# Optimization experiments

Measured on AMD Instinct MI355X. Metric: run time of the kernel, lower is better.

The kernel has to match this reference:

```python
import jax, jax.numpy as jnp
import numpy as np

B, N, M, K = 8, 24000, 6000, 32
C_IN, C_MID, C_OUT = 64, 128, 256  # channels=[64,128,256]; conv input is C_IN+3 (dp_fj)


def setup_inputs() -> dict:
    key = jax.random.key(0)
    ks = jax.random.split(key, 8)
    return {
        "query_xyz": jax.random.normal(ks[0], (B, M, 3), jnp.float32),
        "support_xyz": jax.random.normal(ks[1], (B, N, 3), jnp.float32),
        "features": jax.random.normal(ks[2], (B, C_IN, N), jnp.float32),
        "neighbor_idx": jax.random.randint(ks[3], (B, M, K), 0, N, dtype=jnp.int32),
        "W1": jax.random.normal(ks[4], (C_MID, C_IN + 3), jnp.float32) * 0.05,
        "b1": jnp.zeros((C_MID,), jnp.float32),
        "W2": jax.random.normal(ks[5], (C_OUT, C_MID), jnp.float32) * 0.05,
        "b2": jnp.zeros((C_OUT,), jnp.float32),
    }


def _conv1d_relu(x, W, b):
    # pointwise conv1d (kernel size 1) + bias + ReLU; x: [B, Cin, N]
    return jax.nn.relu(jnp.einsum('oc,bcn->bon', W, x) + b[None, :, None])


def reference(query_xyz, support_xyz, features, neighbor_idx, W1, b1, W2, b2):
    # Delayed aggregation: transform features FIRST (convs on support points),
    # then gather neighbors per query and max-reduce.
    x = jnp.concatenate([features, support_xyz.transpose(0, 2, 1)], axis=1)  # [B, C_IN+3, N]
    x = _conv1d_relu(x, W1, b1)   # [B, C_MID, N]
    x = _conv1d_relu(x, W2, b2)   # [B, C_OUT, N]
    # grouper: gather neighbor features fj = x[b, :, neighbor_idx[b, m, k]] -> [B, C_OUT, M, K]
    idx = jnp.broadcast_to(neighbor_idx.reshape(B, 1, M * K), (B, C_OUT, M * K))
    fj = jnp.take_along_axis(x, idx, axis=2).reshape(B, C_OUT, M, K)
    # reduction_layer: max over neighbor dim
    return jnp.max(fj, axis=-1)  # [B, C_OUT, M]
```

## Files before the change

kernel.cpp:

```cpp
#include <hip/hip_runtime.h>
#include <hip/hip_bf16.h>

typedef unsigned short u16;
typedef short s16x8 __attribute__((ext_vector_type(8)));
typedef float f32x4 __attribute__((ext_vector_type(4)));
typedef unsigned short u16x8 __attribute__((ext_vector_type(8)));

#define B_   8
#define N_   24000
#define M_   6000
#define K_   32
#define CIN  64
#define CMID 128
#define COUT 256
#define KP1  96
#define QB_  188

__device__ __align__(16) u16 g_W1f[CMID * KP1];
__device__ __align__(16) u16 g_W2f[COUT * CMID];
__device__ __align__(16) u16 g_Yf[(size_t)B_ * N_ * COUT];

__device__ __forceinline__ float bf2f(u16 u) {
    return __uint_as_float(((unsigned)u) << 16);
}
__device__ __forceinline__ u16 f2bf(float f) {
    unsigned u = __float_as_uint(f);
    u += 0x7FFFu + ((u >> 16) & 1u);
    return (u16)(u >> 16);
}
__device__ __forceinline__ unsigned f2bf2(float lo, float hi) {
    __hip_bfloat162 h = __float22bfloat162_rn(make_float2(lo, hi));
    unsigned r;
    __builtin_memcpy(&r, &h, 4);
    return r;
}

__global__ void prep_weights(const float* __restrict__ W1,
                             const float* __restrict__ W2) {
    int t = blockIdx.x * 256 + threadIdx.x;
    if (t < CMID * KP1) {
        int blk = t >> 9, off = t & 511;
        int L = off >> 3, j = off & 7;
        int ln = L & 15, quad = L >> 4;
        int w = blk / 6, r = blk % 6;
        int k0i = r >> 1, mt = r & 1;
        int row = w * 32 + mt * 16 + ln;
        int col = k0i * 32 + quad * 8 + j;
        g_W1f[t] = (col < 67) ? f2bf(W1[row * 67 + col]) : (u16)0;
    } else {
        int i = t - CMID * KP1;
        int blk = i >> 9, off = i & 511;
        int L = off >> 3, j = off & 7;
        int ln = L & 15, quad = L >> 4;
        int w = blk >> 4, r = blk & 15;
        int k0i = r >> 2, mt = r & 3;
        int row = w * 64 + mt * 16 + ln;
        int col = k0i * 32 + quad * 8 + j;
        g_W2f[i] = f2bf(W2[row * 128 + col]);
    }
}

__global__ __launch_bounds__(256) void conv_fused(
        const float* __restrict__ feat, const float* __restrict__ xyz,
        const float* __restrict__ b1,  const float* __restrict__ b2) {
    __shared__ __align__(16) u16 sm[16896];
    u16* Xs = sm;
    u16* Hs = sm + 6656;
    u16* Ys = sm;

    const int tid  = threadIdx.x;
    const int b    = blockIdx.y;
    const int n0   = blockIdx.x * 64;
    const int w    = tid >> 6;
    const int L    = tid & 63;
    const int ln   = L & 15;
    const int quad = L >> 4;

    if (tid < 64) {
        uint4 z; z.x = z.y = z.z = z.w = 0u;
        u16* xr = Xs + tid * 104;
        *(uint4*)(xr + 64) = z; *(uint4*)(xr + 72) = z;
        *(uint4*)(xr + 80) = z; *(uint4*)(xr + 88) = z;
        const float* s = xyz + (size_t)(b * N_ + n0 + tid) * 3;
        xr[64] = f2bf(s[0]); xr[65] = f2bf(s[1]); xr[66] = f2bf(s[2]);
    }
#pragma unroll
    for (int it = 0; it < 4; ++it) {
        int idx = it * 256 + tid;
        int c   = idx >> 4;
        int p0  = (idx & 15) << 2;
        float4 v = *(const float4*)(feat + (size_t)(b * CIN + c) * N_ + n0 + p0);
        u16* dst = Xs + p0 * 104 + c;
        unsigned pxy = f2bf2(v.x, v.y);
        unsigned pzw = f2bf2(v.z, v.w);
        dst[0]   = (u16)pxy;
        dst[104] = (u16)(pxy >> 16);
        dst[208] = (u16)pzw;
        dst[312] = (u16)(pzw >> 16);
    }
    __syncthreads();

    f32x4 acc1[2][4];
#pragma unroll
    for (int mt = 0; mt < 2; ++mt)
#pragma unroll
        for (int nt = 0; nt < 4; ++nt) {
            f32x4 zz = {0.f, 0.f, 0.f, 0.f};
            acc1[mt][nt] = zz;
        }
#pragma unroll
    for (int k0i = 0; k0i < 3; ++k0i) {
        s16x8 af[2], xf[4];
#pragma unroll
        for (int mt = 0; mt < 2; ++mt)
            af[mt] = *(const s16x8*)(g_W1f + (((w * 3 + k0i) * 2 + mt) << 9) + L * 8);
#pragma unroll
        for (int nt = 0; nt < 4; ++nt)
            xf[nt] = *(const s16x8*)(Xs + (nt * 16 + ln) * 104 + k0i * 32 + quad * 8);
#pragma unroll
        for (int mt = 0; mt < 2; ++mt)
#pragma unroll
            for (int nt = 0; nt < 4; ++nt)
                acc1[mt][nt] = __builtin_amdgcn_mfma_f32_16x16x32_bf16(
                    af[mt], xf[nt], acc1[mt][nt], 0, 0, 0);
    }
#pragma unroll
    for (int mt = 0; mt < 2; ++mt) {
        int m0 = w * 32 + mt * 16 + quad * 4;
        float4 bv = *(const float4*)(b1 + m0);
#pragma unroll
        for (int nt = 0; nt < 4; ++nt) {
            int p = nt * 16 + ln;
            uint2 hv;
            hv.x = f2bf2(fmaxf(acc1[mt][nt][0] + bv.x, 0.f),
                         fmaxf(acc1[mt][nt][1] + bv.y, 0.f));
            hv.y = f2bf2(fmaxf(acc1[mt][nt][2] + bv.z, 0.f),
                         fmaxf(acc1[mt][nt][3] + bv.w, 0.f));
            *(uint2*)(Hs + p * 136 + m0) = hv;
        }
    }
    __syncthreads();

    f32x4 acc2[4][4];
#pragma unroll
    for (int mt = 0; mt < 4; ++mt)
#pragma unroll
        for (int nt = 0; nt < 4; ++nt) {
            f32x4 zz = {0.f, 0.f, 0.f, 0.f};
            acc2[mt][nt] = zz;
        }
#pragma unroll
    for (int k0i = 0; k0i < 4; ++k0i) {
        s16x8 af[4], hf[4];
#pragma unroll
        for (int mt = 0; mt < 4; ++mt)
            af[mt] = *(const s16x8*)(g_W2f + (((w * 4 + k0i) * 4 + mt) << 9) + L * 8);
#pragma unroll
        for (int nt = 0; nt < 4; ++nt)
            hf[nt] = *(const s16x8*)(Hs + (nt * 16 + ln) * 136 + k0i * 32 + quad * 8);
#pragma unroll
        for (int mt = 0; mt < 4; ++mt)
#pragma unroll
            for (int nt = 0; nt < 4; ++nt)
                acc2[mt][nt] = __builtin_amdgcn_mfma_f32_16x16x32_bf16(
                    af[mt], hf[nt], acc2[mt][nt], 0, 0, 0);
    }
    __syncthreads();

#pragma unroll
    for (int mt = 0; mt < 4; ++mt) {
        int c0 = w * 64 + mt * 16 + quad * 4;
        float4 bv = *(const float4*)(b2 + c0);
#pragma unroll
        for (int nt = 0; nt < 4; ++nt) {
            int p = nt * 16 + ln;
            uint2 yv;
            yv.x = f2bf2(fmaxf(acc2[mt][nt][0] + bv.x, 0.f),
                         fmaxf(acc2[mt][nt][1] + bv.y, 0.f));
            yv.y = f2bf2(fmaxf(acc2[mt][nt][2] + bv.z, 0.f),
                         fmaxf(acc2[mt][nt][3] + bv.w, 0.f));
            *(uint2*)(Ys + p * 264 + c0) = yv;
        }
    }
    __syncthreads();

    u16* dstY = g_Yf + ((size_t)b * N_ + n0) * COUT;
#pragma unroll
    for (int i = 0; i < 8; ++i) {
        int g = i * 256 + tid;
        int p = g >> 5, c16 = g & 31;
        *(uint4*)(dstY + (size_t)p * COUT + c16 * 8) =
            *(const uint4*)(Ys + p * 264 + c16 * 8);
    }
}

__global__ __launch_bounds__(256) void gather_max(
        const int* __restrict__ nbr, float* __restrict__ out) {
    __shared__ __align__(16) u16 smem[32 * 400];
    int* sidx  = (int*)smem;
    u16* ssort = smem + 2048;
    int* soff  = (int*)(smem + 3072);
    int* scur  = (int*)(smem + 3328);
    u16* ymax  = smem;

    const int tid = threadIdx.x;
    const int l   = blockIdx.x;
    const int xcd = l & 7;
    const int j   = l >> 3;
    const int cw  = j / QB_;
    const int qb  = j % QB_;
    const int combo = cw * 8 + xcd;
    const int b   = combo >> 2;
    const int q   = combo & 3;
    const int m0  = qb * 32;
    const int row = tid >> 3;
    const int Mv0 = M_ - m0;
    const int Mv  = Mv0 < 32 ? Mv0 : 32;

    if (row < Mv)
        *(int4*)(sidx + tid * 4) =
            *(const int4*)(nbr + ((size_t)b * M_ + m0) * K_ + tid * 4);
    if (tid < 128) scur[tid] = 0;
    __syncthreads();

    unsigned uu[4];
#pragma unroll
    for (int jj = 0; jj < 4; ++jj) {
        unsigned u = (unsigned)sidx[tid * 4 + jj];
        u = u < (unsigned)N_ ? u : 0u;
        uu[jj] = u;
        int p = (int)(u >> 13);
        if (p < 2) atomicAdd(&scur[row * 4 + p], 1);
    }
    __syncthreads();

    if (tid < 32) {
        int c0 = scur[tid * 4 + 0], c1 = scur[tid * 4 + 1];
        soff[tid * 4 + 0] = 0;
        soff[tid * 4 + 1] = c0;
        soff[tid * 4 + 2] = c0 + c1;
        soff[tid * 4 + 3] = 32;
        scur[tid * 4 + 0] = 0;
        scur[tid * 4 + 1] = c0;
        scur[tid * 4 + 2] = c0 + c1;
    }
    __syncthreads();

#pragma unroll
    for (int jj = 0; jj < 4; ++jj) {
        int p = (int)(uu[jj] >> 13);
        int pos = atomicAdd(&scur[row * 4 + p], 1);
        ssort[row * 32 + pos] = (u16)uu[jj];
    }
    __syncthreads();

    const int w  = tid >> 6;
    const int L  = tid & 63;
    const int kg = L >> 3;
    const int co = L & 7;
    const u16* base = g_Yf + (size_t)b * N_ * COUT + q * 64 + co * 8;

    u16x8 mx[8];
#pragma unroll
    for (int i = 0; i < 8; ++i)
        mx[i] = (u16x8){0, 0, 0, 0, 0, 0, 0, 0};

#pragma unroll
    for (int p = 0; p < 3; ++p) {
#pragma unroll
        for (int h = 0; h < 2; ++h) {
            int mq[4], beg[4], end[4], last[4];
            u16x8 va[4], vb[4];
#pragma unroll
            for (int s = 0; s < 4; ++s) {
                int ml = w * 8 + h * 4 + s;
                mq[s]  = ml < Mv ? ml : 0;
                beg[s] = soff[mq[s] * 4 + p];
                end[s] = soff[mq[s] * 4 + p + 1];
                int lt = end[s] - 1;
                last[s] = lt > 0 ? lt : 0;
                int p0 = beg[s] + kg; p0 = p0 < last[s] ? p0 : last[s];
                unsigned i0 = (unsigned)ssort[mq[s] * 32 + p0];
                va[s] = *(const u16x8*)(base + (size_t)i0 * COUT);
            }
#pragma unroll
            for (int s = 0; s < 4; ++s) {
                int p1 = beg[s] + 8 + kg; p1 = p1 < last[s] ? p1 : last[s];
                unsigned i1 = (unsigned)ssort[mq[s] * 32 + p1];
                vb[s] = *(const u16x8*)(base + (size_t)i1 * COUT);
            }
#pragma unroll
            for (int s = 0; s < 4; ++s)
                mx[h * 4 + s] = __builtin_elementwise_max(mx[h * 4 + s],
                    __builtin_elementwise_max(va[s], vb[s]));
#pragma unroll
            for (int s = 0; s < 4; ++s) {
                for (int r = beg[s] + 16; r < end[s]; r += 8) {
                    int pp = r + kg; pp = pp < last[s] ? pp : last[s];
                    unsigned ii = (unsigned)ssort[mq[s] * 32 + pp];
                    u16x8 vv = *(const u16x8*)(base + (size_t)ii * COUT);
                    mx[h * 4 + s] = __builtin_elementwise_max(mx[h * 4 + s], vv);
                }
            }
        }
    }

    __syncthreads();

#pragma unroll
    for (int i = 0; i < 8; ++i) {
        int ml = w * 8 + i;
        if (ml < Mv) {
            u16x8 m8 = mx[i];
#pragma unroll
            for (int mask = 8; mask <= 32; mask <<= 1) {
                int4 t = *(int4*)&m8;
                t.x = __shfl_xor(t.x, mask);
                t.y = __shfl_xor(t.y, mask);
                t.z = __shfl_xor(t.z, mask);
                t.w = __shfl_xor(t.w, mask);
                m8 = __builtin_elementwise_max(m8, *(u16x8*)&t);
            }
            if (kg == 0)
                *(u16x8*)(ymax + ml * 400 + co * 8) = m8;
        }
    }
    __syncthreads();

    int valid = Mv;
#pragma unroll
    for (int it = 0; it < 2; ++it) {
        int c  = it * 32 + (tid >> 3);
        int mc = (tid & 7) << 2;
        if (mc + 4 <= valid) {
            float4 v;
            v.x = bf2f(ymax[(mc + 0) * 400 + c]);
            v.y = bf2f(ymax[(mc + 1) * 400 + c]);
            v.z = bf2f(ymax[(mc + 2) * 400 + c]);
            v.w = bf2f(ymax[(mc + 3) * 400 + c]);
            *(float4*)(out + (size_t)(b * COUT + q * 64 + c) * M_ + m0 + mc) = v;
        }
    }
}

extern "C" void kernel_launch(void* const* d_in, const int* in_sizes, int n_in,
                              void* d_out, int out_size, void* d_ws, size_t ws_size,
                              hipStream_t stream) {
    const float* xyz  = (const float*)d_in[1];
    const float* feat = (const float*)d_in[2];
    const int*   nbr  = (const int*)d_in[3];
    const float* W1   = (const float*)d_in[4];
    const float* b1   = (const float*)d_in[5];
    const float* W2   = (const float*)d_in[6];
    const float* b2   = (const float*)d_in[7];
    float* out = (float*)d_out;
    (void)d_ws; (void)ws_size;

    prep_weights<<<176, 256, 0, stream>>>(W1, W2);
    conv_fused<<<dim3(N_ / 64, B_), 256, 0, stream>>>(feat, xyz, b1, b2);
    gather_max<<<32 * QB_, 256, 0, stream>>>(nbr, out);
}
```

Measured before the change: 253.2 us.

## Process three point tiles per conv block with register-prefetched next tile

The fused conv kernel now runs 125 blocks per batch, each handling three 64-point tiles in a loop. Each thread loads its 16 channels of raw features for the next tile into registers while the MFMA work on the current tile runs, hiding global load latency. The shared-memory transpose store is also reorganized so each thread writes contiguous 16-channel vectors. The cost is fewer blocks in flight (1000 vs 3000), more register pressure and extra barriers per tile.

```diff
diff --git a/kernel.cpp b/kernel.cpp
--- a/kernel.cpp
+++ b/kernel.cpp
@@ -70,127 +70,158 @@
 
     const int tid  = threadIdx.x;
     const int b    = blockIdx.y;
-    const int n0   = blockIdx.x * 64;
     const int w    = tid >> 6;
     const int L    = tid & 63;
     const int ln   = L & 15;
     const int quad = L >> 4;
-
-    if (tid < 64) {
-        uint4 z; z.x = z.y = z.z = z.w = 0u;
-        u16* xr = Xs + tid * 104;
-        *(uint4*)(xr + 64) = z; *(uint4*)(xr + 72) = z;
-        *(uint4*)(xr + 80) = z; *(uint4*)(xr + 88) = z;
-        const float* s = xyz + (size_t)(b * N_ + n0 + tid) * 3;
-        xr[64] = f2bf(s[0]); xr[65] = f2bf(s[1]); xr[66] = f2bf(s[2]);
-    }
-#pragma unroll
-    for (int it = 0; it < 4; ++it) {
-        int idx = it * 256 + tid;
-        int c   = idx >> 4;
-        int p0  = (idx & 15) << 2;
-        float4 v = *(const float4*)(feat + (size_t)(b * CIN + c) * N_ + n0 + p0);
-        u16* dst = Xs + p0 * 104 + c;
-        unsigned pxy = f2bf2(v.x, v.y);
-        unsigned pzw = f2bf2(v.z, v.w);
-        dst[0]   = (u16)pxy;
-        dst[104] = (u16)(pxy >> 16);
-        dst[208] = (u16)pzw;
-        dst[312] = (u16)(pzw >> 16);
-    }
-    __syncthreads();
-
-    f32x4 acc1[2][4];
-#pragma unroll
-    for (int mt = 0; mt < 2; ++mt)
-#pragma unroll
-        for (int nt = 0; nt < 4; ++nt) {
-            f32x4 zz = {0.f, 0.f, 0.f, 0.f};
-            acc1[mt][nt] = zz;
-        }
-#pragma unroll
-    for (int k0i = 0; k0i < 3; ++k0i) {
-        s16x8 af[2], xf[4];
+    const int p    = L;
+    const int cg   = w;
+
+    const float* fbase = feat + (size_t)(b * CIN + cg * 16) * N_;
+
+    float raw[16];
+    float px = 0.f, py = 0.f, pz = 0.f;
+
+    {
+        const int n0 = blockIdx.x * 192;
+#pragma unroll
+        for (int jj = 0; jj < 16; ++jj)
+            raw[jj] = fbase[(size_t)jj * N_ + n0 + p];
+        if (cg == 0) {
+            const float* s = xyz + (size_t)(b * N_ + n0 + p) * 3;
+            px = s[0]; py = s[1]; pz = s[2];
+        }
+    }
+
+    for (int t = 0; t < 3; ++t) {
+        const int n0 = blockIdx.x * 192 + t * 64;
+
+        {
+            u16* dst = Xs + p * 104 + cg * 16;
+            uint4 w0, w1;
+            w0.x = f2bf2(raw[0],  raw[1]);  w0.y = f2bf2(raw[2],  raw[3]);
+            w0.z = f2bf2(raw[4],  raw[5]);  w0.w = f2bf2(raw[6],  raw[7]);
+            w1.x = f2bf2(raw[8],  raw[9]);  w1.y = f2bf2(raw[10], raw[11]);
+            w1.z = f2bf2(raw[12], raw[13]); w1.w = f2bf2(raw[14], raw[15]);
+            *(uint4*)dst = w0;
+            *(uint4*)(dst + 8) = w1;
+            if (cg == 0) {
+                u16* xr = Xs + p * 104 + 64;
+                uint4 z4; z4.x = f2bf2(px, py); z4.y = f2bf2(pz, 0.f);
+                z4.z = 0u; z4.w = 0u;
+                uint4 zz; zz.x = zz.y = zz.z = zz.w = 0u;
+                *(uint4*)xr = z4;
+                *(uint4*)(xr + 8)  = zz;
+                *(uint4*)(xr + 16) = zz;
+                *(uint4*)(xr + 24) = zz;
+            }
+        }
+        __syncthreads();
+
+        if (t < 2) {
+            const int n1 = n0 + 64;
+#pragma unroll
+            for (int jj = 0; jj < 16; ++jj)
+                raw[jj] = fbase[(size_t)jj * N_ + n1 + p];
+            if (cg == 0) {
+                const float* s = xyz + (size_t)(b * N_ + n1 + p) * 3;
+                px = s[0]; py = s[1]; pz = s[2];
+            }
+        }
+
+        f32x4 acc1[2][4];
 #pragma unroll
         for (int mt = 0; mt < 2; ++mt)
-            af[mt] = *(const s16x8*)(g_W1f + (((w * 3 + k0i) * 2 + mt) << 9) + L * 8);
-#pragma unroll
-        for (int nt = 0; nt < 4; ++nt)
-            xf[nt] = *(const s16x8*)(Xs + (nt * 16 + ln) * 104 + k0i * 32 + quad * 8);
-#pragma unroll
-        for (int mt = 0; mt < 2; ++mt)
+#pragma unroll
+            for (int nt = 0; nt < 4; ++nt) {
+                f32x4 zz = {0.f, 0.f, 0.f, 0.f};
+                acc1[mt][nt] = zz;
+            }
+#pragma unroll
+        for (int k0i = 0; k0i < 3; ++k0i) {
+            s16x8 af[2], xf[4];
+#pragma unroll
+            for (int mt = 0; mt < 2; ++mt)
+                af[mt] = *(const s16x8*)(g_W1f + (((w * 3 + k0i) * 2 + mt) << 9) + L * 8);
 #pragma unroll
             for (int nt = 0; nt < 4; ++nt)
-                acc1[mt][nt] = __builtin_amdgcn_mfma_f32_16x16x32_bf16(
-                    af[mt], xf[nt], acc1[mt][nt], 0, 0, 0);
-    }
-#pragma unroll
-    for (int mt = 0; mt < 2; ++mt) {
-        int m0 = w * 32 + mt * 16 + quad * 4;
-        float4 bv = *(const float4*)(b1 + m0);
-#pragma unroll
-        for (int nt = 0; nt < 4; ++nt) {
-            int p = nt * 16 + ln;
-            uint2 hv;
-            hv.x = f2bf2(fmaxf(acc1[mt][nt][0] + bv.x, 0.f),
-                         fmaxf(acc1[mt][nt][1] + bv.y, 0.f));
-            hv.y = f2bf2(fmaxf(acc1[mt][nt][2] + bv.z, 0.f),
-                         fmaxf(acc1[mt][nt][3] + bv.w, 0.f));
-            *(uint2*)(Hs + p * 136 + m0) = hv;
-        }
-    }
-    __syncthreads();
-
-    f32x4 acc2[4][4];
-#pragma unroll
-    for (int mt = 0; mt < 4; ++mt)
-#pragma unroll
-        for (int nt = 0; nt < 4; ++nt) {
-            f32x4 zz = {0.f, 0.f, 0.f, 0.f};
-            acc2[mt][nt] = zz;
-        }
-#pragma unroll
-    for (int k0i = 0; k0i < 4; ++k0i) {
-        s16x8 af[4], hf[4];
+                xf[nt] = *(const s16x8*)(Xs + (nt * 16 + ln) * 104 + k0i * 32 + quad * 8);
+#pragma unroll
+            for (int mt = 0; mt < 2; ++mt)
+#pragma unroll
+                for (int nt = 0; nt < 4; ++nt)
+                    acc1[mt][nt] = __builtin_amdgcn_mfma_f32_16x16x32_bf16(
+                        af[mt], xf[nt], acc1[mt][nt], 0, 0, 0);
+        }
+#pragma unroll
+        for (int mt = 0; mt < 2; ++mt) {
+            int m0 = w * 32 + mt * 16 + quad * 4;
+            float4 bv = *(const float4*)(b1 + m0);
+#pragma unroll
+            for (int nt = 0; nt < 4; ++nt) {
+                int pp = nt * 16 + ln;
+                uint2 hv;
+                hv.x = f2bf2(fmaxf(acc1[mt][nt][0] + bv.x, 0.f),
+                             fmaxf(acc1[mt][nt][1] + bv.y, 0.f));
+                hv.y = f2bf2(fmaxf(acc1[mt][nt][2] + bv.z, 0.f),
+                             fmaxf(acc1[mt][nt][3] + bv.w, 0.f));
+                *(uint2*)(Hs + pp * 136 + m0) = hv;
+            }
+        }
+        __syncthreads();
+
+        f32x4 acc2[4][4];
 #pragma unroll
         for (int mt = 0; mt < 4; ++mt)
-            af[mt] = *(const s16x8*)(g_W2f + (((w * 4 + k0i) * 4 + mt) << 9) + L * 8);
-#pragma unroll
-        for (int nt = 0; nt < 4; ++nt)
-            hf[nt] = *(const s16x8*)(Hs + (nt * 16 + ln) * 136 + k0i * 32 + quad * 8);
-#pragma unroll
-        for (int mt = 0; mt < 4; ++mt)
+#pragma unroll
+            for (int nt = 0; nt < 4; ++nt) {
+                f32x4 zz = {0.f, 0.f, 0.f, 0.f};
+                acc2[mt][nt] = zz;
+            }
+#pragma unroll
+        for (int k0i = 0; k0i < 4; ++k0i) {
+            s16x8 af[4], hf[4];
+#pragma unroll
+            for (int mt = 0; mt < 4; ++mt)
+                af[mt] = *(const s16x8*)(g_W2f + (((w * 4 + k0i) * 4 + mt) << 9) + L * 8);
 #pragma unroll
             for (int nt = 0; nt < 4; ++nt)
-                acc2[mt][nt] = __builtin_amdgcn_mfma_f32_16x16x32_bf16(
-                    af[mt], hf[nt], acc2[mt][nt], 0, 0, 0);
-    }
-    __syncthreads();
-
-#pragma unroll
-    for (int mt = 0; mt < 4; ++mt) {
-        int c0 = w * 64 + mt * 16 + quad * 4;
-        float4 bv = *(const float4*)(b2 + c0);
-#pragma unroll
-        for (int nt = 0; nt < 4; ++nt) {
-            int p = nt * 16 + ln;
-            uint2 yv;
-            yv.x = f2bf2(fmaxf(acc2[mt][nt][0] + bv.x, 0.f),
-                         fmaxf(acc2[mt][nt][1] + bv.y, 0.f));
-            yv.y = f2bf2(fmaxf(acc2[mt][nt][2] + bv.z, 0.f),
-                         fmaxf(acc2[mt][nt][3] + bv.w, 0.f));
-            *(uint2*)(Ys + p * 264 + c0) = yv;
-        }
-    }
-    __syncthreads();
-
-    u16* dstY = g_Yf + ((size_t)b * N_ + n0) * COUT;
-#pragma unroll
-    for (int i = 0; i < 8; ++i) {
-        int g = i * 256 + tid;
-        int p = g >> 5, c16 = g & 31;
-        *(uint4*)(dstY + (size_t)p * COUT + c16 * 8) =
-            *(const uint4*)(Ys + p * 264 + c16 * 8);
+                hf[nt] = *(const s16x8*)(Hs + (nt * 16 + ln) * 136 + k0i * 32 + quad * 8);
+#pragma unroll
+            for (int mt = 0; mt < 4; ++mt)
+#pragma unroll
+                for (int nt = 0; nt < 4; ++nt)
+                    acc2[mt][nt] = __builtin_amdgcn_mfma_f32_16x16x32_bf16(
+                        af[mt], hf[nt], acc2[mt][nt], 0, 0, 0);
+        }
+        __syncthreads();
+
+#pragma unroll
+        for (int mt = 0; mt < 4; ++mt) {
+            int c0 = w * 64 + mt * 16 + quad * 4;
+            float4 bv = *(const float4*)(b2 + c0);
+#pragma unroll
+            for (int nt = 0; nt < 4; ++nt) {
+                int pp = nt * 16 + ln;
+                uint2 yv;
+                yv.x = f2bf2(fmaxf(acc2[mt][nt][0] + bv.x, 0.f),
+                             fmaxf(acc2[mt][nt][1] + bv.y, 0.f));
+                yv.y = f2bf2(fmaxf(acc2[mt][nt][2] + bv.z, 0.f),
+                             fmaxf(acc2[mt][nt][3] + bv.w, 0.f));
+                *(uint2*)(Ys + pp * 264 + c0) = yv;
+            }
+        }
+        __syncthreads();
+
+        u16* dstY = g_Yf + ((size_t)b * N_ + n0) * COUT;
+#pragma unroll
+        for (int i = 0; i < 8; ++i) {
+            int g = i * 256 + tid;
+            int pp = g >> 5, c16 = g & 31;
+            *(uint4*)(dstY + (size_t)pp * COUT + c16 * 8) =
+                *(const uint4*)(Ys + pp * 264 + c16 * 8);
+        }
+        if (t < 2) __syncthreads();
     }
 }
 
@@ -229,8 +260,8 @@
         unsigned u = (unsigned)sidx[tid * 4 + jj];
         u = u < (unsigned)N_ ? u : 0u;
         uu[jj] = u;
-        int p = (int)(u >> 13);
-        if (p < 2) atomicAdd(&scur[row * 4 + p], 1);
+        int pp = (int)(u >> 13);
+        if (pp < 2) atomicAdd(&scur[row * 4 + pp], 1);
     }
     __syncthreads();
 
@@ -248,8 +279,8 @@
 
 #pragma unroll
     for (int jj = 0; jj < 4; ++jj) {
-        int p = (int)(uu[jj] >> 13);
-        int pos = atomicAdd(&scur[row * 4 + p], 1);
+        int pp = (int)(uu[jj] >> 13);
+        int pos = atomicAdd(&scur[row * 4 + pp], 1);
         ssort[row * 32 + pos] = (u16)uu[jj];
     }
     __syncthreads();
@@ -296,8 +327,8 @@
 #pragma unroll
             for (int s = 0; s < 4; ++s) {
                 for (int r = beg[s] + 16; r < end[s]; r += 8) {
-                    int pp = r + kg; pp = pp < last[s] ? pp : last[s];
-                    unsigned ii = (unsigned)ssort[mq[s] * 32 + pp];
+                    int pq = r + kg; pq = pq < last[s] ? pq : last[s];
+                    unsigned ii = (unsigned)ssort[mq[s] * 32 + pq];
                     u16x8 vv = *(const u16x8*)(base + (size_t)ii * COUT);
                     mx[h * 4 + s] = __builtin_elementwise_max(mx[h * 4 + s], vv);
                 }
@@ -357,6 +388,6 @@
     (void)d_ws; (void)ws_size;
 
     prep_weights<<<176, 256, 0, stream>>>(W1, W2);
-    conv_fused<<<dim3(N_ / 64, B_), 256, 0, stream>>>(feat, xyz, b1, b2);
+    conv_fused<<<dim3(125, B_), 256, 0, stream>>>(feat, xyz, b1, b2);
     gather_max<<<32 * QB_, 256, 0, stream>>>(nbr, out);
 }
```

Result: no change. 249.2 us (-1.6%).
